# Optimization experiments

Measured on AMD Instinct MI355X. Metric: run time of the kernel, lower is better.

## Reference

```python
import jax, jax.numpy as jnp
import numpy as np


def setup_inputs() -> dict:
    key = jax.random.key(0)
    k_x, k_q, k_k, k_v = jax.random.split(key, 4)
    B, S, F, U = 8, 2048, 1024, 256
    x = jax.random.normal(k_x, (B, S, F), dtype=jnp.float32)
    Wq = jax.random.normal(k_q, (F, U), dtype=jnp.float32) * 0.05
    Wk = jax.random.normal(k_k, (F, U), dtype=jnp.float32) * 0.05
    Wv = jax.random.normal(k_v, (F, U), dtype=jnp.float32) * 0.05
    return {"x": x, "Wq": Wq, "Wk": Wk, "Wv": Wv}


def reference(x, Wq, Wk, Wv):
    # x: [B, S, F]; projections tanh-activated: [B, S, U]
    xQ = jnp.tanh(jnp.einsum("bsf,fu->bsu", x, Wq))
    xK = jnp.tanh(jnp.einsum("bsf,fu->bsu", x, Wk))
    xV = jnp.tanh(jnp.einsum("bsf,fu->bsu", x, Wv))
    scale = 1.0 / jnp.sqrt(jnp.asarray(x.shape[-1], dtype=jnp.float32))
    scores = jnp.einsum("bsu,btu->bst", xQ, xK) * scale  # [B, S, S]
    weights = jax.nn.softmax(scores, axis=-1)
    out = jnp.einsum("bst,btu->bsu", weights, xV)  # return_sequences=True
    return out
```

## Files before the change

kernel.cpp:

```cpp
#include <hip/hip_runtime.h>
#include <math.h>

#define B_ 8
#define S_ 2048
#define F_ 1024
#define U_ 256
#define M_ (B_ * S_)

typedef __attribute__((ext_vector_type(8))) short bf16x8;
typedef __attribute__((ext_vector_type(4))) float f32x4;
typedef __attribute__((ext_vector_type(16))) float f32x16;
typedef unsigned short ushort_t;

__device__ __forceinline__ unsigned short f2bf(float x) {
    unsigned u = __builtin_bit_cast(unsigned, x);
    unsigned r = (u + 0x7fffu + ((u >> 16) & 1u)) >> 16;
    return (unsigned short)r;
}
__device__ __forceinline__ float bf2f(unsigned short b) {
    return __builtin_bit_cast(float, ((unsigned)b) << 16);
}
__device__ __forceinline__ void gload16(const void* g, void* l) {
    __builtin_amdgcn_global_load_lds(
        (const __attribute__((address_space(1))) unsigned int*)g,
        (__attribute__((address_space(3))) unsigned int*)l, 16, 0, 0);
}
__device__ __forceinline__ f32x4 zero4() {
    f32x4 v; v[0] = 0.f; v[1] = 0.f; v[2] = 0.f; v[3] = 0.f; return v;
}

__global__ __launch_bounds__(256) void convxt_kernel(
    const float* __restrict__ x, ushort_t* __restrict__ xbt)
{
    __shared__ ushort_t T[8][129][8];

    const int t  = threadIdx.x;
    const int r0 = blockIdx.x * 128;
    const int k0 = blockIdx.y * 64;

    #pragma unroll
    for (int i = 0; i < 8; ++i) {
        const int r = i * 16 + (t >> 4);
        const int c = (t & 15) * 4;
        const float4 v = *reinterpret_cast<const float4*>(
            x + (size_t)(r0 + r) * F_ + k0 + c);
        ushort4 o;
        o.x = f2bf(v.x); o.y = f2bf(v.y); o.z = f2bf(v.z); o.w = f2bf(v.w);
        *reinterpret_cast<ushort4*>(&T[c >> 3][r][c & 7]) = o;
    }
    __syncthreads();
    #pragma unroll
    for (int i = 0; i < 4; ++i) {
        const int ci  = i * 256 + t;
        const int ksl = ci >> 7, r = ci & 127;
        ushort_t* dst = xbt + ((size_t)(blockIdx.y * 8 + ksl) * M_ + r0 + r) * 8;
        *reinterpret_cast<bf16x8*>(dst) =
            *reinterpret_cast<const bf16x8*>(&T[ksl][r][0]);
    }
}

__global__ __launch_bounds__(256) void convw_kernel(
    const float* __restrict__ Wq, const float* __restrict__ Wk,
    const float* __restrict__ Wv, ushort_t* __restrict__ Wp)
{
    const int ks   = blockIdx.x;
    const int wsel = blockIdx.y;
    const float* __restrict__ W = (wsel == 0) ? Wq : (wsel == 1) ? Wk : Wv;
    const int n = threadIdx.x;

    bf16x8 hv, lv;
    #pragma unroll
    for (int j = 0; j < 8; ++j) {
        float v = W[(size_t)(ks * 8 + j) * U_ + n];
        ushort_t h = f2bf(v);
        hv[j] = (short)h;
        lv[j] = (short)f2bf(v - bf2f(h));
    }
    size_t base = (size_t)wsel * 524288;
    *reinterpret_cast<bf16x8*>(&Wp[base + ((size_t)ks) * 2048 + n * 8]) = hv;
    *reinterpret_cast<bf16x8*>(&Wp[base + ((size_t)(128 + ks)) * 2048 + n * 8]) = lv;
}

__global__ __launch_bounds__(256, 2) void proj_mfma_kernel(
    const ushort_t* __restrict__ xbt,
    const ushort_t* __restrict__ Wp,
    ushort_t* __restrict__ qh_g, ushort_t* __restrict__ kh_g,
    ushort_t* __restrict__ vth_g)
{
    __shared__ ushort_t As[4][2 * 128 * 8];
    __shared__ ushort_t Bs[3][2 * 2 * 256 * 8];

    const int orig = blockIdx.x;
    const int xcd  = orig & 7;
    const int idx  = orig >> 3;
    const int q3   = idx / 3;
    const int wsel = idx - q3 * 3;
    const int row0 = (xcd * 16 + q3) * 128;

    const int tid = threadIdx.x;
    const int l = tid & 63, w = tid >> 6;
    const int m = l & 31, hi = l >> 5;

    const ushort_t* __restrict__ WpB = Wp + (size_t)wsel * 524288;

    f32x16 acc[4][2];
    #pragma unroll
    for (int mr = 0; mr < 4; ++mr)
        #pragma unroll
        for (int nf = 0; nf < 2; ++nf)
            #pragma unroll
            for (int r = 0; r < 16; ++r) acc[mr][nf][r] = 0.f;

    auto stageA = [&](int buf, int ks) {
        const int ksl = tid >> 7, r = tid & 127;
        const ushort_t* src = xbt + ((size_t)(ks * 2 + ksl) * M_ + row0 + r) * 8;
        gload16(src, (char*)&As[buf][0] + (size_t)(w * 64) * 16);
    };
    auto stageB = [&](int buf, int ks) {
        #pragma unroll
        for (int i = 0; i < 4; ++i) {
            const int ci = i * 256 + tid;
            const int half = ci >> 9, rem = ci & 511;
            const int ksl = rem >> 8, n = rem & 255;
            const ushort_t* src = WpB + (size_t)half * 262144
                                  + (size_t)(ks * 2 + ksl) * 2048 + n * 8;
            gload16(src, (char*)&Bs[buf][0] + (size_t)(i * 256 + w * 64) * 16);
        }
    };

    stageA(0, 0);
    stageB(0, 0);
    stageA(1, 1);
    stageB(1, 1);
    stageA(2, 2);

    for (int ks = 0; ks < 64; ++ks) {
        if (ks < 62) asm volatile("s_waitcnt vmcnt(6)" ::: "memory");
        else         asm volatile("s_waitcnt vmcnt(0)" ::: "memory");
        __builtin_amdgcn_s_barrier();
        if (ks + 2 < 64) stageB((ks + 2) % 3, ks + 2);
        if (ks + 3 < 64) stageA((ks + 3) & 3, ks + 3);

        const ushort_t* Ac = &As[ks & 3][0];
        const ushort_t* Bc = &Bs[ks % 3][0];

        bf16x8 ah[4];
        #pragma unroll
        for (int mr = 0; mr < 4; ++mr)
            ah[mr] = *reinterpret_cast<const bf16x8*>(
                &Ac[(size_t)(hi * 128 + mr * 32 + m) * 8]);
        bf16x8 bh[2], bl[2];
        #pragma unroll
        for (int nf = 0; nf < 2; ++nf) {
            const int nn = w * 64 + nf * 32 + m;
            bh[nf] = *reinterpret_cast<const bf16x8*>(
                &Bc[(size_t)(hi * 256 + nn) * 8]);
            bl[nf] = *reinterpret_cast<const bf16x8*>(
                &Bc[(size_t)(512 + hi * 256 + nn) * 8]);
        }
        #pragma unroll
        for (int nf = 0; nf < 2; ++nf)
            #pragma unroll
            for (int mr = 0; mr < 4; ++mr)
                acc[mr][nf] = __builtin_amdgcn_mfma_f32_32x32x16_bf16(
                    ah[mr], bh[nf], acc[mr][nf], 0, 0, 0);
        #pragma unroll
        for (int nf = 0; nf < 2; ++nf)
            #pragma unroll
            for (int mr = 0; mr < 4; ++mr)
                acc[mr][nf] = __builtin_amdgcn_mfma_f32_32x32x16_bf16(
                    ah[mr], bl[nf], acc[mr][nf], 0, 0, 0);
    }

    #pragma unroll
    for (int mr = 0; mr < 4; ++mr) {
        const int row_base = row0 + mr * 32;
        if (wsel < 2) {
            ushort_t* __restrict__ hp = (wsel == 0) ? qh_g : kh_g;
            #pragma unroll
            for (int nf = 0; nf < 2; ++nf) {
                const int u = w * 64 + nf * 32 + m;
                #pragma unroll
                for (int reg = 0; reg < 16; ++reg) {
                    const int rl = (reg & 3) + 8 * (reg >> 2) + 4 * hi;
                    hp[(size_t)(row_base + rl) * U_ + u] =
                        f2bf(tanhf(acc[mr][nf][reg]));
                }
            }
        } else {
            const int b     = row0 >> 11;
            const int s_blk = (row0 & 2047) + mr * 32;
            #pragma unroll
            for (int nf = 0; nf < 2; ++nf) {
                const int u = w * 64 + nf * 32 + m;
                #pragma unroll
                for (int rg = 0; rg < 4; ++rg) {
                    ushort4 hv;
                    hv.x = f2bf(tanhf(acc[mr][nf][rg * 4 + 0]));
                    hv.y = f2bf(tanhf(acc[mr][nf][rg * 4 + 1]));
                    hv.z = f2bf(tanhf(acc[mr][nf][rg * 4 + 2]));
                    hv.w = f2bf(tanhf(acc[mr][nf][rg * 4 + 3]));
                    size_t off = ((size_t)b * U_ + u) * S_ + s_blk + 8 * rg + 4 * hi;
                    *reinterpret_cast<ushort4*>(&vth_g[off]) = hv;
                }
            }
        }
    }
}

__global__ __launch_bounds__(256, 2) void attn_mfma_kernel(
    const ushort_t* __restrict__ qh_g,
    const ushort_t* __restrict__ kh_g,
    const ushort_t* __restrict__ vth_g,
    float* __restrict__ O0, float* __restrict__ O1,
    float* __restrict__ ml)
{
    __shared__ ushort_t Kbuf[2][32 * 256];
    __shared__ ushort_t Vbuf[2][256 * 40];
    __shared__ ushort_t Pbuf[4][512];

    const int tid = threadIdx.x;
    const int l  = tid & 63, w = tid >> 6;
    const int kq = l & 15,  g = l >> 4;

    const int logical = (blockIdx.x & 7) * 64 + (blockIdx.x >> 3);
    const int b     = logical >> 6;
    const int qb    = (logical >> 1) & 31;
    const int khalf = logical & 1;
    const int qrow0 = b * S_ + qb * 64 + w * 16;
    const int kb0   = khalf * 1024;

    bf16x8 qh[8];
    {
        const ushort_t* qbh = qh_g + (size_t)(qrow0 + kq) * U_;
        #pragma unroll
        for (int us = 0; us < 8; ++us)
            qh[us] = *reinterpret_cast<const bf16x8*>(qbh + us * 32 + g * 8);
    }

    f32x4 O[16];
    #pragma unroll
    for (int nt = 0; nt < 16; ++nt) O[nt] = zero4();
    float m_run = -INFINITY, l_run = 0.f;

    auto stage = [&](int buf, int k0) {
        #pragma unroll
        for (int i = 0; i < 4; ++i) {
            int c = w * 256 + i * 64 + l;
            int key = c >> 5, uc = c & 31;
            int ucs = uc ^ (key & 7);
            size_t so = (size_t)(b * S_ + k0 + key) * U_ + ucs * 8;
            gload16(kh_g + so, &Kbuf[buf][(w * 256 + i * 64) * 8]);
        }
        #pragma unroll
        for (int i = 0; i < 5; ++i) {
            int c = w * 320 + i * 64 + l;
            int u = (c * 52429) >> 18;
            int kc = c - u * 5;
            size_t so = ((size_t)b * U_ + u) * S_ + k0 + kc * 8;
            const ushort_t* sh = (kc < 4) ? (vth_g + so) : vth_g;
            gload16(sh, &Vbuf[buf][(w * 320 + i * 64) * 8]);
        }
    };

    stage(0, kb0);

    const float scale = 0.03125f;

    for (int t = 0; t < 32; ++t) {
        const int cur = t & 1;
        asm volatile("s_waitcnt vmcnt(0)" ::: "memory");
        __builtin_amdgcn_s_barrier();
        if (t < 31) stage(cur ^ 1, kb0 + (t + 1) * 32);

        const ushort_t* Kh = Kbuf[cur];
        const ushort_t* Vh = Vbuf[cur];

        f32x4 hh0 = zero4(), hh1 = zero4();
        #pragma unroll
        for (int us = 0; us < 8; ++us) {
            int off0 = kq * 256 + ((us * 32 + g * 8) ^ ((kq & 7) * 8));
            bf16x8 k0h = *reinterpret_cast<const bf16x8*>(Kh + off0);
            hh0 = __builtin_amdgcn_mfma_f32_16x16x32_bf16(k0h, qh[us], hh0, 0, 0, 0);
            int off1 = off0 + 16 * 256;
            bf16x8 k1h = *reinterpret_cast<const bf16x8*>(Kh + off1);
            hh1 = __builtin_amdgcn_mfma_f32_16x16x32_bf16(k1h, qh[us], hh1, 0, 0, 0);
        }
        f32x4 s0 = hh0 * scale;
        f32x4 s1 = hh1 * scale;

        float tm = fmaxf(fmaxf(fmaxf(s0[0], s0[1]), fmaxf(s0[2], s0[3])),
                         fmaxf(fmaxf(s1[0], s1[1]), fmaxf(s1[2], s1[3])));
        tm = fmaxf(tm, __shfl_xor(tm, 16));
        tm = fmaxf(tm, __shfl_xor(tm, 32));
        float mn = fmaxf(m_run, tm);
        ushort_t ph0[4], ph1[4];
        float su = 0.f;
        #pragma unroll
        for (int r = 0; r < 4; ++r) {
            ph0[r] = f2bf(expf(s0[r] - mn)); su += bf2f(ph0[r]);
        }
        #pragma unroll
        for (int r = 0; r < 4; ++r) {
            ph1[r] = f2bf(expf(s1[r] - mn)); su += bf2f(ph1[r]);
        }
        su += __shfl_xor(su, 16);
        su += __shfl_xor(su, 32);
        float f = expf(m_run - mn);
        l_run = l_run * f + su;
        m_run = mn;

        {
            ushort4 a, c;
            a.x = ph0[0]; a.y = ph0[1]; a.z = ph0[2]; a.w = ph0[3];
            c.x = ph1[0]; c.y = ph1[1]; c.z = ph1[2]; c.w = ph1[3];
            int pw0 = ((g >> 1)) * 128 + kq * 8 + (g & 1) * 4;
            int pw1 = (2 + (g >> 1)) * 128 + kq * 8 + (g & 1) * 4;
            *reinterpret_cast<ushort4*>(&Pbuf[w][pw0]) = a;
            *reinterpret_cast<ushort4*>(&Pbuf[w][pw1]) = c;
        }

        float fr0 = __shfl(f, g * 4 + 0), fr1 = __shfl(f, g * 4 + 1);
        float fr2 = __shfl(f, g * 4 + 2), fr3 = __shfl(f, g * 4 + 3);
        #pragma unroll
        for (int nt = 0; nt < 16; ++nt) {
            O[nt][0] *= fr0; O[nt][1] *= fr1; O[nt][2] *= fr2; O[nt][3] *= fr3;
        }

        bf16x8 pa_h = *reinterpret_cast<const bf16x8*>(&Pbuf[w][g * 128 + kq * 8]);
        #pragma unroll
        for (int nt = 0; nt < 16; ++nt) {
            int vo = (nt * 16 + kq) * 40 + g * 8;
            bf16x8 vh = *reinterpret_cast<const bf16x8*>(Vh + vo);
            O[nt] = __builtin_amdgcn_mfma_f32_16x16x32_bf16(pa_h, vh, O[nt], 0, 0, 0);
        }
    }

    float* __restrict__ Op = khalf ? O1 : O0;
    #pragma unroll
    for (int nt = 0; nt < 16; ++nt) {
        const int col = nt * 16 + kq;
        Op[(size_t)(qrow0 + g * 4 + 0) * U_ + col] = O[nt][0];
        Op[(size_t)(qrow0 + g * 4 + 1) * U_ + col] = O[nt][1];
        Op[(size_t)(qrow0 + g * 4 + 2) * U_ + col] = O[nt][2];
        Op[(size_t)(qrow0 + g * 4 + 3) * U_ + col] = O[nt][3];
    }
    if (g == 0) {
        ml[((size_t)khalf * M_ + qrow0 + kq) * 2 + 0] = m_run;
        ml[((size_t)khalf * M_ + qrow0 + kq) * 2 + 1] = l_run;
    }
}

__global__ __launch_bounds__(256) void merge_kernel(
    const float* __restrict__ O1, const float* __restrict__ ml,
    float* __restrict__ out)
{
    const int tid = threadIdx.x;
    const int row = blockIdx.x * 4 + (tid >> 6);
    const int c   = (tid & 63) * 4;

    const float m0 = ml[(size_t)row * 2 + 0];
    const float l0 = ml[(size_t)row * 2 + 1];
    const float m1 = ml[((size_t)M_ + row) * 2 + 0];
    const float l1 = ml[((size_t)M_ + row) * 2 + 1];
    const float Mx = fmaxf(m0, m1);
    float a0 = expf(m0 - Mx), a1 = expf(m1 - Mx);
    const float inv = 1.f / (a0 * l0 + a1 * l1);
    a0 *= inv; a1 *= inv;

    const size_t off = (size_t)row * U_ + c;
    const float4 o0 = *reinterpret_cast<const float4*>(out + off);
    const float4 o1 = *reinterpret_cast<const float4*>(O1 + off);
    float4 r;
    r.x = o0.x * a0 + o1.x * a1;
    r.y = o0.y * a0 + o1.y * a1;
    r.z = o0.z * a0 + o1.z * a1;
    r.w = o0.w * a0 + o1.w * a1;
    *reinterpret_cast<float4*>(out + off) = r;
}

extern "C" void kernel_launch(void* const* d_in, const int* in_sizes, int n_in,
                              void* d_out, int out_size, void* d_ws, size_t ws_size,
                              hipStream_t stream)
{
    (void)in_sizes; (void)n_in; (void)out_size; (void)ws_size;
    const float* x  = (const float*)d_in[0];
    const float* Wq = (const float*)d_in[1];
    const float* Wk = (const float*)d_in[2];
    const float* Wv = (const float*)d_in[3];
    float* out = (float*)d_out;

    ushort_t* ws = (ushort_t*)d_ws;
    const size_t T = (size_t)M_ * U_;
    ushort_t* qh_g  = ws;
    ushort_t* kh_g  = ws + T;
    ushort_t* vth_g = ws + 2 * T;
    ushort_t* Wp    = ws + 3 * T;
    ushort_t* xbt   = ws + 3 * T + 1572864;
    float*    O1    = (float*)xbt;
    float*    ml    = O1 + T;

    convxt_kernel<<<dim3(128, 16), 256, 0, stream>>>(x, xbt);
    convw_kernel<<<dim3(128, 3), 256, 0, stream>>>(Wq, Wk, Wv, Wp);

    proj_mfma_kernel<<<dim3(384), 256, 0, stream>>>(
        xbt, Wp, qh_g, kh_g, vth_g);

    attn_mfma_kernel<<<dim3(512), 256, 0, stream>>>(
        qh_g, kh_g, vth_g, out, O1, ml);

    merge_kernel<<<dim3(M_ / 4), 256, 0, stream>>>(O1, ml, out);
}
```

Measured before the change: 179.4 us.

## Retile projection GEMM to 128x128 blocks and defer softmax rescaling in attention

```diff
diff --git a/kernel.cpp b/kernel.cpp
--- a/kernel.cpp
+++ b/kernel.cpp
@@ -81,105 +81,114 @@
     *reinterpret_cast<bf16x8*>(&Wp[base + ((size_t)(128 + ks)) * 2048 + n * 8]) = lv;
 }
 
-__global__ __launch_bounds__(256, 2) void proj_mfma_kernel(
+__global__ __launch_bounds__(256, 3) void proj_mfma_kernel(
     const ushort_t* __restrict__ xbt,
     const ushort_t* __restrict__ Wp,
     ushort_t* __restrict__ qh_g, ushort_t* __restrict__ kh_g,
     ushort_t* __restrict__ vth_g)
 {
-    __shared__ ushort_t As[4][2 * 128 * 8];
-    __shared__ ushort_t Bs[3][2 * 2 * 256 * 8];
+    __shared__ ushort_t As[2][4 * 128 * 8];
+    __shared__ ushort_t Bs[2][2 * 4 * 128 * 8];
 
     const int orig = blockIdx.x;
     const int xcd  = orig & 7;
-    const int idx  = orig >> 3;
-    const int q3   = idx / 3;
-    const int wsel = idx - q3 * 3;
-    const int row0 = (xcd * 16 + q3) * 128;
+    const int i    = orig >> 3;
+    const int rt6  = i / 6;
+    const int sub  = i - rt6 * 6;
+    const int wsel = sub >> 1;
+    const int nh   = sub & 1;
+    const int row0 = (xcd * 16 + rt6) * 128;
+    const int col0 = nh * 128;
 
     const int tid = threadIdx.x;
     const int l = tid & 63, w = tid >> 6;
+    const int wy = w >> 1, wx = w & 1;
     const int m = l & 31, hi = l >> 5;
 
     const ushort_t* __restrict__ WpB = Wp + (size_t)wsel * 524288;
 
-    f32x16 acc[4][2];
-    #pragma unroll
-    for (int mr = 0; mr < 4; ++mr)
+    f32x16 acc[2][2];
+    #pragma unroll
+    for (int mr = 0; mr < 2; ++mr)
         #pragma unroll
         for (int nf = 0; nf < 2; ++nf)
             #pragma unroll
             for (int r = 0; r < 16; ++r) acc[mr][nf][r] = 0.f;
 
     auto stageA = [&](int buf, int ks) {
-        const int ksl = tid >> 7, r = tid & 127;
-        const ushort_t* src = xbt + ((size_t)(ks * 2 + ksl) * M_ + row0 + r) * 8;
-        gload16(src, (char*)&As[buf][0] + (size_t)(w * 64) * 16);
+        #pragma unroll
+        for (int it = 0; it < 2; ++it) {
+            const int ci = it * 256 + tid;
+            const int ksl = ci >> 7, r = ci & 127;
+            const ushort_t* src =
+                xbt + ((size_t)(ks * 4 + ksl) * M_ + row0 + r) * 8;
+            gload16(src, (char*)&As[buf][0] + (size_t)(it * 256 + w * 64) * 16);
+        }
     };
     auto stageB = [&](int buf, int ks) {
         #pragma unroll
-        for (int i = 0; i < 4; ++i) {
-            const int ci = i * 256 + tid;
-            const int half = ci >> 9, rem = ci & 511;
-            const int ksl = rem >> 8, n = rem & 255;
+        for (int it = 0; it < 4; ++it) {
+            const int ci = it * 256 + tid;
+            const int half = ci >> 9, ksl = (ci >> 7) & 3, n = ci & 127;
             const ushort_t* src = WpB + (size_t)half * 262144
-                                  + (size_t)(ks * 2 + ksl) * 2048 + n * 8;
-            gload16(src, (char*)&Bs[buf][0] + (size_t)(i * 256 + w * 64) * 16);
+                                  + (size_t)(ks * 4 + ksl) * 2048
+                                  + (size_t)(col0 + n) * 8;
+            gload16(src, (char*)&Bs[buf][0] + (size_t)(it * 256 + w * 64) * 16);
         }
     };
 
     stageA(0, 0);
     stageB(0, 0);
-    stageA(1, 1);
-    stageB(1, 1);
-    stageA(2, 2);
-
-    for (int ks = 0; ks < 64; ++ks) {
-        if (ks < 62) asm volatile("s_waitcnt vmcnt(6)" ::: "memory");
-        else         asm volatile("s_waitcnt vmcnt(0)" ::: "memory");
-        __builtin_amdgcn_s_barrier();
-        if (ks + 2 < 64) stageB((ks + 2) % 3, ks + 2);
-        if (ks + 3 < 64) stageA((ks + 3) & 3, ks + 3);
-
-        const ushort_t* Ac = &As[ks & 3][0];
-        const ushort_t* Bc = &Bs[ks % 3][0];
-
-        bf16x8 ah[4];
-        #pragma unroll
-        for (int mr = 0; mr < 4; ++mr)
-            ah[mr] = *reinterpret_cast<const bf16x8*>(
-                &Ac[(size_t)(hi * 128 + mr * 32 + m) * 8]);
-        bf16x8 bh[2], bl[2];
-        #pragma unroll
-        for (int nf = 0; nf < 2; ++nf) {
-            const int nn = w * 64 + nf * 32 + m;
-            bh[nf] = *reinterpret_cast<const bf16x8*>(
-                &Bc[(size_t)(hi * 256 + nn) * 8]);
-            bl[nf] = *reinterpret_cast<const bf16x8*>(
-                &Bc[(size_t)(512 + hi * 256 + nn) * 8]);
-        }
-        #pragma unroll
-        for (int nf = 0; nf < 2; ++nf)
-            #pragma unroll
-            for (int mr = 0; mr < 4; ++mr)
-                acc[mr][nf] = __builtin_amdgcn_mfma_f32_32x32x16_bf16(
-                    ah[mr], bh[nf], acc[mr][nf], 0, 0, 0);
-        #pragma unroll
-        for (int nf = 0; nf < 2; ++nf)
-            #pragma unroll
-            for (int mr = 0; mr < 4; ++mr)
-                acc[mr][nf] = __builtin_amdgcn_mfma_f32_32x32x16_bf16(
-                    ah[mr], bl[nf], acc[mr][nf], 0, 0, 0);
-    }
-
-    #pragma unroll
-    for (int mr = 0; mr < 4; ++mr) {
-        const int row_base = row0 + mr * 32;
+    __syncthreads();
+
+    for (int ks = 0; ks < 32; ++ks) {
+        const int cur = ks & 1;
+        if (ks < 31) { stageA(cur ^ 1, ks + 1); stageB(cur ^ 1, ks + 1); }
+
+        const ushort_t* Ac = &As[cur][0];
+        const ushort_t* Bc = &Bs[cur][0];
+
+        #pragma unroll
+        for (int g = 0; g < 2; ++g) {
+            const int ksl = g * 2 + hi;
+            bf16x8 ah[2];
+            #pragma unroll
+            for (int mr = 0; mr < 2; ++mr)
+                ah[mr] = *reinterpret_cast<const bf16x8*>(
+                    &Ac[(size_t)(ksl * 128 + wy * 64 + mr * 32 + m) * 8]);
+            bf16x8 bh[2], bl[2];
+            #pragma unroll
+            for (int nf = 0; nf < 2; ++nf) {
+                const int nn = wx * 64 + nf * 32 + m;
+                bh[nf] = *reinterpret_cast<const bf16x8*>(
+                    &Bc[(size_t)(ksl * 128 + nn) * 8]);
+                bl[nf] = *reinterpret_cast<const bf16x8*>(
+                    &Bc[(size_t)(512 * 8 + (ksl * 128 + nn) * 8)]);
+            }
+            #pragma unroll
+            for (int nf = 0; nf < 2; ++nf)
+                #pragma unroll
+                for (int mr = 0; mr < 2; ++mr)
+                    acc[mr][nf] = __builtin_amdgcn_mfma_f32_32x32x16_bf16(
+                        ah[mr], bh[nf], acc[mr][nf], 0, 0, 0);
+            #pragma unroll
+            for (int nf = 0; nf < 2; ++nf)
+                #pragma unroll
+                for (int mr = 0; mr < 2; ++mr)
+                    acc[mr][nf] = __builtin_amdgcn_mfma_f32_32x32x16_bf16(
+                        ah[mr], bl[nf], acc[mr][nf], 0, 0, 0);
+        }
+        __syncthreads();
+    }
+
+    #pragma unroll
+    for (int mr = 0; mr < 2; ++mr) {
+        const int row_base = row0 + wy * 64 + mr * 32;
         if (wsel < 2) {
             ushort_t* __restrict__ hp = (wsel == 0) ? qh_g : kh_g;
             #pragma unroll
             for (int nf = 0; nf < 2; ++nf) {
-                const int u = w * 64 + nf * 32 + m;
+                const int u = col0 + wx * 64 + nf * 32 + m;
                 #pragma unroll
                 for (int reg = 0; reg < 16; ++reg) {
                     const int rl = (reg & 3) + 8 * (reg >> 2) + 4 * hi;
@@ -189,10 +198,10 @@
             }
         } else {
             const int b     = row0 >> 11;
-            const int s_blk = (row0 & 2047) + mr * 32;
+            const int s_blk = (row0 & 2047) + wy * 64 + mr * 32;
             #pragma unroll
             for (int nf = 0; nf < 2; ++nf) {
-                const int u = w * 64 + nf * 32 + m;
+                const int u = col0 + wx * 64 + nf * 32 + m;
                 #pragma unroll
                 for (int rg = 0; rg < 4; ++rg) {
                     ushort4 hv;
@@ -293,22 +302,27 @@
                          fmaxf(fmaxf(s1[0], s1[1]), fmaxf(s1[2], s1[3])));
         tm = fmaxf(tm, __shfl_xor(tm, 16));
         tm = fmaxf(tm, __shfl_xor(tm, 32));
-        float mn = fmaxf(m_run, tm);
+        const bool defer = __all(tm - m_run <= 4.0f);
+        float mn, f;
+        if (defer) {
+            mn = m_run;
+        } else {
+            mn = fmaxf(m_run, tm);
+            f = __expf(m_run - mn);
+            m_run = mn;
+        }
         ushort_t ph0[4], ph1[4];
         float su = 0.f;
         #pragma unroll
         for (int r = 0; r < 4; ++r) {
-            ph0[r] = f2bf(expf(s0[r] - mn)); su += bf2f(ph0[r]);
+            ph0[r] = f2bf(__expf(s0[r] - mn)); su += bf2f(ph0[r]);
         }
         #pragma unroll
         for (int r = 0; r < 4; ++r) {
-            ph1[r] = f2bf(expf(s1[r] - mn)); su += bf2f(ph1[r]);
+            ph1[r] = f2bf(__expf(s1[r] - mn)); su += bf2f(ph1[r]);
         }
         su += __shfl_xor(su, 16);
         su += __shfl_xor(su, 32);
-        float f = expf(m_run - mn);
-        l_run = l_run * f + su;
-        m_run = mn;
 
         {
             ushort4 a, c;
@@ -320,11 +334,17 @@
             *reinterpret_cast<ushort4*>(&Pbuf[w][pw1]) = c;
         }
 
-        float fr0 = __shfl(f, g * 4 + 0), fr1 = __shfl(f, g * 4 + 1);
-        float fr2 = __shfl(f, g * 4 + 2), fr3 = __shfl(f, g * 4 + 3);
-        #pragma unroll
-        for (int nt = 0; nt < 16; ++nt) {
-            O[nt][0] *= fr0; O[nt][1] *= fr1; O[nt][2] *= fr2; O[nt][3] *= fr3;
+        if (defer) {
+            l_run += su;
+        } else {
+            l_run = l_run * f + su;
+            float fr0 = __shfl(f, g * 4 + 0), fr1 = __shfl(f, g * 4 + 1);
+            float fr2 = __shfl(f, g * 4 + 2), fr3 = __shfl(f, g * 4 + 3);
+            #pragma unroll
+            for (int nt = 0; nt < 16; ++nt) {
+                O[nt][0] *= fr0; O[nt][1] *= fr1;
+                O[nt][2] *= fr2; O[nt][3] *= fr3;
+            }
         }
 
         bf16x8 pa_h = *reinterpret_cast<const bf16x8*>(&Pbuf[w][g * 128 + kq * 8]);
@@ -403,7 +423,7 @@
     convxt_kernel<<<dim3(128, 16), 256, 0, stream>>>(x, xbt);
     convw_kernel<<<dim3(128, 3), 256, 0, stream>>>(Wq, Wk, Wv, Wp);
 
-    proj_mfma_kernel<<<dim3(384), 256, 0, stream>>>(
+    proj_mfma_kernel<<<dim3(768), 256, 0, stream>>>(
         xbt, Wp, qh_g, kh_g, vth_g);
 
     attn_mfma_kernel<<<dim3(512), 256, 0, stream>>>(
```

Result: faster. 160.2 us (-10.7%).
